# Performance work log

Measured on AMD Instinct MI355X. Metric: run time of the kernel, lower is better.

Reference implementation:

```python
import jax, jax.numpy as jnp
import numpy as np

D_EMB = 256
SCALE = 0.02
B, T = 4, 4096
EPS = 1e-5


def layer_norm(x, w, b):
    m = jnp.mean(x, axis=-1, keepdims=True)
    v = jnp.mean((x - m) ** 2, axis=-1, keepdims=True)
    return (x - m) * jax.lax.rsqrt(v + EPS) * w + b


def setup_inputs() -> dict:
    key = jax.random.key(0)
    ks = jax.random.split(key, 4)
    x = jax.random.normal(ks[0], (B, T, D_EMB), dtype=jnp.float32)
    qkv = jax.random.normal(ks[1], (3, D_EMB, D_EMB), dtype=jnp.float32) * SCALE
    # nn.Linear(D, 2D, bias=False): weight shape (2D, D), applied as x @ W.T
    w1 = jax.random.normal(ks[2], (2 * D_EMB, D_EMB), dtype=jnp.float32) * (1.0 / np.sqrt(D_EMB))
    w2 = jax.random.normal(ks[3], (D_EMB, 2 * D_EMB), dtype=jnp.float32) * (1.0 / np.sqrt(2 * D_EMB))
    ones = jnp.ones((D_EMB,), dtype=jnp.float32)
    zeros = jnp.zeros((D_EMB,), dtype=jnp.float32)
    return {
        "x": x, "qkv": qkv,
        "ln_q_w": ones, "ln_q_b": zeros,
        "ln_k_w": ones, "ln_k_b": zeros,
        "ln_attn_w": ones, "ln_attn_b": zeros,
        "w1": w1, "w2": w2,
        "ln_ff_w": ones, "ln_ff_b": zeros,
    }


def reference(x, qkv, ln_q_w, ln_q_b, ln_k_w, ln_k_b, ln_attn_w, ln_attn_b, w1, w2, ln_ff_w, ln_ff_b):
    # QKV projections: [3, B, T, D]
    y = jnp.einsum('btd,ndD->nbtD', x, qkv)
    q, k, v = y[0], y[1], y[2]
    q = layer_norm(q, ln_q_w, ln_q_b)
    k = layer_norm(k, ln_k_w, ln_k_b)
    # full (non-causal) single-head attention, scale by sqrt(D_EMB)
    scores = jnp.einsum('btd,bsd->bts', q, k) / jnp.sqrt(jnp.float32(D_EMB))
    attn = jax.nn.softmax(scores, axis=-1)
    y = jnp.einsum('bts,bsd->btd', attn, v)
    y = layer_norm(y, ln_attn_w, ln_attn_b)
    x = 0.7 * (x + y)
    # FFN with dual leaky_relu
    y = jax.nn.leaky_relu(x @ w1.T, negative_slope=0.2)
    y = jax.nn.leaky_relu(y @ w2.T, negative_slope=0.2)
    y = layer_norm(y, ln_ff_w, ln_ff_b)
    return 0.7 * (x + y)
```

## Files before the change

### kernel.cpp

```cpp
#include <hip/hip_runtime.h>

#define BSZ   4
#define TSEQ  4096
#define DEMB  256
#define NTOK  (BSZ * TSEQ)
#define HID   512
#define SPLITS 4
#define KEYS_PER_SPLIT (TSEQ / SPLITS)
#define TK 32
#define NT (KEYS_PER_SPLIT / TK)
#define KIMG_STRIDE 8704
#define VIMG_STRIDE 10240

using bf16x8 = __attribute__((ext_vector_type(8))) short;
using f32x16 = __attribute__((ext_vector_type(16))) float;

static __device__ __forceinline__ unsigned short f2bf(float f) {
  union { float f; unsigned u; } v; v.f = f;
  unsigned r = v.u + 0x7FFF + ((v.u >> 16) & 1);
  return (unsigned short)(r >> 16);
}
static __device__ __forceinline__ float bf2f(unsigned short u) {
  union { unsigned u; float f; } v; v.u = ((unsigned)u) << 16;
  return v.f;
}

static __device__ __forceinline__ void async16(void* lds, const void* gp) {
  __builtin_amdgcn_global_load_lds(
      (const __attribute__((address_space(1))) unsigned int*)gp,
      (__attribute__((address_space(3))) unsigned int*)lds, 16, 0, 0);
}

__global__ __launch_bounds__(256) void prep_kernel(
    const float* __restrict__ qkv, const float* __restrict__ w1,
    const float* __restrict__ w2, unsigned short* __restrict__ qkvT,
    unsigned short* __restrict__ w1b, unsigned short* __restrict__ w2b)
{
  const int tid = threadIdx.x;
  if (blockIdx.y < 3) {
    if (blockIdx.x >= 16) return;
    __shared__ float Ts[64][65];
    const int z  = blockIdx.y;
    const int k0 = (blockIdx.x >> 2) * 64;
    const int j0 = (blockIdx.x & 3) * 64;
    const float* src = qkv + (size_t)z * DEMB * DEMB + (size_t)k0 * DEMB + j0;
#pragma unroll
    for (int p = 0; p < 4; ++p) {
      int idx = p * 256 + tid;
      int r = idx >> 4, g = idx & 15;
      float4 v = *(const float4*)(src + (size_t)r * DEMB + g * 4);
      Ts[r][g * 4 + 0] = v.x; Ts[r][g * 4 + 1] = v.y;
      Ts[r][g * 4 + 2] = v.z; Ts[r][g * 4 + 3] = v.w;
    }
    __syncthreads();
    unsigned short* dst = qkvT + (size_t)z * DEMB * DEMB + (size_t)j0 * DEMB + k0;
#pragma unroll
    for (int p = 0; p < 4; ++p) {
      int idx = p * 256 + tid;
      int r = idx >> 4, g = idx & 15;
      ushort4 o;
      o.x = f2bf(Ts[g * 4 + 0][r]); o.y = f2bf(Ts[g * 4 + 1][r]);
      o.z = f2bf(Ts[g * 4 + 2][r]); o.w = f2bf(Ts[g * 4 + 3][r]);
      *(ushort4*)(dst + (size_t)r * DEMB + g * 4) = o;
    }
  } else {
    const float* s = (blockIdx.y == 3) ? w1 : w2;
    unsigned short* d = (blockIdx.y == 3) ? w1b : w2b;
    const int i = blockIdx.x * 256 + tid;
    float4 v = ((const float4*)s)[i];
    ushort4 o;
    o.x = f2bf(v.x); o.y = f2bf(v.y); o.z = f2bf(v.z); o.w = f2bf(v.w);
    ((ushort4*)d)[i] = o;
  }
}

__global__ __launch_bounds__(512, 1) void qkvln_kernel(
    const float* __restrict__ x, const unsigned short* __restrict__ qkvT,
    const float* __restrict__ lnqw, const float* __restrict__ lnqb,
    const float* __restrict__ lnkw, const float* __restrict__ lnkb,
    unsigned short* __restrict__ Qbn, unsigned short* __restrict__ Kimg,
    unsigned short* __restrict__ Vimg)
{
  __shared__ __align__(16) unsigned short sh[36864];
  unsigned short* As = sh;
  unsigned short* Bs = sh + 256 * 72;

  const int tid = threadIdx.x;
  const int w   = tid >> 6;
  const int l   = tid & 63;
  const int lm  = l & 31;
  const int lh  = l >> 5;
  const int z   = blockIdx.y;
  const int m0  = blockIdx.x * 256;
  const int bb  = m0 >> 12;

  const unsigned short* Bt = qkvT + (size_t)z * DEMB * DEMB;

  f32x16 o[8];
#pragma unroll
  for (int t = 0; t < 8; ++t)
#pragma unroll
    for (int r = 0; r < 16; ++r) o[t][r] = 0.f;

  const int fr = tid >> 4;
  const int fc = (tid & 15) * 4;

  float4 arf[8];
  bf16x8 brb[4];

#pragma unroll
  for (int i = 0; i < 8; ++i)
    arf[i] = *(const float4*)(x + (size_t)(m0 + fr + 32 * i) * DEMB + fc);
#pragma unroll
  for (int i = 0; i < 4; ++i) {
    const int c = tid + 512 * i;
    brb[i] = *(const bf16x8*)(Bt + (size_t)(c >> 3) * DEMB + (c & 7) * 8);
  }

  for (int k0 = 0; k0 < DEMB; k0 += 64) {
    __syncthreads();
#pragma unroll
    for (int i = 0; i < 8; ++i) {
      ushort4 u;
      u.x = f2bf(arf[i].x); u.y = f2bf(arf[i].y);
      u.z = f2bf(arf[i].z); u.w = f2bf(arf[i].w);
      *(ushort4*)&As[(fr + 32 * i) * 72 + fc] = u;
    }
#pragma unroll
    for (int i = 0; i < 4; ++i) {
      const int c = tid + 512 * i;
      *(bf16x8*)&Bs[(c >> 3) * 72 + (c & 7) * 8] = brb[i];
    }
    __syncthreads();

    if (k0 + 64 < DEMB) {
      const int kn = k0 + 64;
#pragma unroll
      for (int i = 0; i < 8; ++i)
        arf[i] = *(const float4*)(x + (size_t)(m0 + fr + 32 * i) * DEMB + kn + fc);
#pragma unroll
      for (int i = 0; i < 4; ++i) {
        const int c = tid + 512 * i;
        brb[i] = *(const bf16x8*)(Bt + (size_t)(c >> 3) * DEMB + kn + (c & 7) * 8);
      }
    }

#pragma unroll
    for (int ks = 0; ks < 4; ++ks) {
      bf16x8 a = *(const bf16x8*)&As[(w * 32 + lm) * 72 + ks * 16 + lh * 8];
#pragma unroll
      for (int t = 0; t < 8; ++t) {
        bf16x8 b = *(const bf16x8*)&Bs[(t * 32 + lm) * 72 + ks * 16 + lh * 8];
        o[t] = __builtin_amdgcn_mfma_f32_32x32x16_bf16(a, b, o[t], 0, 0, 0);
      }
    }
  }

  __syncthreads();

  if (z < 2) {
    const float* wp = z ? lnkw : lnqw;
    const float* bp = z ? lnkb : lnqb;
    float wc[8], bc[8];
#pragma unroll
    for (int t = 0; t < 8; ++t) { wc[t] = wp[t * 32 + lm]; bc[t] = bp[t * 32 + lm]; }
#pragma unroll
    for (int r = 0; r < 16; ++r) {
      float sv = 0.f, sq = 0.f;
#pragma unroll
      for (int t = 0; t < 8; ++t) { const float v = o[t][r]; sv += v; sq += v * v; }
#pragma unroll
      for (int d = 1; d < 32; d <<= 1) { sv += __shfl_xor(sv, d, 64); sq += __shfl_xor(sq, d, 64); }
      const float mean = sv * (1.f / DEMB);
      const float rs = rsqrtf(sq * (1.f / DEMB) - mean * mean + 1e-5f);
      const int token = m0 + w * 32 + (r & 3) + 8 * (r >> 2) + 4 * lh;
      if (z == 0) {
        unsigned short* dst = Qbn + (size_t)token * DEMB;
#pragma unroll
        for (int t = 0; t < 8; ++t)
          dst[t * 32 + lm] = f2bf((o[t][r] - mean) * rs * wc[t] + bc[t]);
      } else {
        const int t5 = token & 4095;
        unsigned short* dst =
            Kimg + (size_t)(bb * 128 + (t5 >> 5)) * KIMG_STRIDE + (t5 & 31) * 264;
#pragma unroll
        for (int t = 0; t < 8; ++t)
          dst[t * 32 + lm] = f2bf((o[t][r] - mean) * rs * wc[t] + bc[t]);
      }
    }
  } else {
#pragma unroll
    for (int h = 0; h < 2; ++h) {
      if (h) __syncthreads();
#pragma unroll
      for (int t2 = 0; t2 < 4; ++t2) {
        const int t = h * 4 + t2;
#pragma unroll
        for (int r = 0; r < 16; ++r) {
          const int row = w * 32 + (r & 3) + 8 * (r >> 2) + 4 * lh;
          sh[row * 130 + t2 * 32 + lm] = f2bf(o[t][r]);
        }
      }
      __syncthreads();
      const int d2 = tid & 127;
      const int tq = tid >> 7;
      const int d  = h * 128 + d2;
#pragma unroll
      for (int j = 0; j < 16; ++j) {
        const int tok0 = tq * 64 + j * 4;
        ushort4 v;
        v.x = sh[(tok0 + 0) * 130 + d2];
        v.y = sh[(tok0 + 1) * 130 + d2];
        v.z = sh[(tok0 + 2) * 130 + d2];
        v.w = sh[(tok0 + 3) * 130 + d2];
        const int gtok = m0 + tok0;
        const int kt = (gtok & 4095) >> 5;
        *(ushort4*)(Vimg + (size_t)(bb * 128 + kt) * VIMG_STRIDE + d * 40 + (tok0 & 31)) = v;
      }
    }
  }
}

__global__ __launch_bounds__(256, 3) void gemm_ffn_kernel(
    const unsigned short* __restrict__ A, const unsigned short* __restrict__ Bt,
    unsigned short* __restrict__ C, int M, int N, int K)
{
  __shared__ __align__(16) unsigned short As[128 * 72];
  __shared__ __align__(16) unsigned short Bs[128 * 72];

  const int tid = threadIdx.x;
  const int w   = tid >> 6;
  const int wm  = w >> 1, wn = w & 1;
  const int l   = tid & 63;
  const int lm  = l & 31;
  const int lh  = l >> 5;

  const int m0    = blockIdx.x * 128;
  const int nbase = blockIdx.y * 128;

  f32x16 acc00, acc01, acc10, acc11;
#pragma unroll
  for (int r = 0; r < 16; ++r) { acc00[r] = 0.f; acc01[r] = 0.f; acc10[r] = 0.f; acc11[r] = 0.f; }

  const int lr = tid >> 3;
  const int lc = (tid & 7) * 8;

  bf16x8 arb[4], brb[4];

#pragma unroll
  for (int i = 0; i < 4; ++i) {
    arb[i] = *(const bf16x8*)(A  + (size_t)(m0 + i * 32 + lr) * K + lc);
    brb[i] = *(const bf16x8*)(Bt + (size_t)(nbase + i * 32 + lr) * K + lc);
  }

  for (int k0 = 0; k0 < K; k0 += 64) {
    __syncthreads();
#pragma unroll
    for (int i = 0; i < 4; ++i) {
      *(bf16x8*)&As[(i * 32 + lr) * 72 + lc] = arb[i];
      *(bf16x8*)&Bs[(i * 32 + lr) * 72 + lc] = brb[i];
    }
    __syncthreads();

    if (k0 + 64 < K) {
      const int kn = k0 + 64;
#pragma unroll
      for (int i = 0; i < 4; ++i) {
        arb[i] = *(const bf16x8*)(A  + (size_t)(m0 + i * 32 + lr) * K + kn + lc);
        brb[i] = *(const bf16x8*)(Bt + (size_t)(nbase + i * 32 + lr) * K + kn + lc);
      }
    }

#pragma unroll
    for (int ks = 0; ks < 4; ++ks) {
      bf16x8 a0 = *(const bf16x8*)&As[(wm * 64 + lm)      * 72 + ks * 16 + lh * 8];
      bf16x8 a1 = *(const bf16x8*)&As[(wm * 64 + 32 + lm) * 72 + ks * 16 + lh * 8];
      bf16x8 b0 = *(const bf16x8*)&Bs[(wn * 64 + lm)      * 72 + ks * 16 + lh * 8];
      bf16x8 b1 = *(const bf16x8*)&Bs[(wn * 64 + 32 + lm) * 72 + ks * 16 + lh * 8];
      acc00 = __builtin_amdgcn_mfma_f32_32x32x16_bf16(a0, b0, acc00, 0, 0, 0);
      acc01 = __builtin_amdgcn_mfma_f32_32x32x16_bf16(a0, b1, acc01, 0, 0, 0);
      acc10 = __builtin_amdgcn_mfma_f32_32x32x16_bf16(a1, b0, acc10, 0, 0, 0);
      acc11 = __builtin_amdgcn_mfma_f32_32x32x16_bf16(a1, b1, acc11, 0, 0, 0);
    }
  }

  const f32x16* accs[4] = { &acc00, &acc01, &acc10, &acc11 };
#pragma unroll
  for (int am = 0; am < 2; ++am)
#pragma unroll
    for (int bn = 0; bn < 2; ++bn) {
      const f32x16& a = *accs[am * 2 + bn];
#pragma unroll
      for (int r = 0; r < 16; ++r) {
        const int m = m0 + wm * 64 + am * 32 + (r & 3) + 8 * (r >> 2) + 4 * lh;
        const int n = nbase + wn * 64 + bn * 32 + lm;
        float v = a[r];
        v = v > 0.f ? v : 0.2f * v;
        C[(size_t)m * N + n] = f2bf(v);
      }
    }
}

__global__ __launch_bounds__(256) void ln_res_bf16_kernel(
    const unsigned short* __restrict__ Y, const float* __restrict__ Xin,
    const float* __restrict__ w, const float* __restrict__ b,
    float* __restrict__ Out)
{
  const int lane = threadIdx.x & 63;
  const size_t row = (size_t)blockIdx.x * 4 + (threadIdx.x >> 6);
  ushort4 u = *(const ushort4*)&Y[row * DEMB + lane * 4];
  float y0 = bf2f(u.x), y1 = bf2f(u.y), y2 = bf2f(u.z), y3 = bf2f(u.w);
  float s  = y0 + y1 + y2 + y3;
  float sq = y0 * y0 + y1 * y1 + y2 * y2 + y3 * y3;
#pragma unroll
  for (int o = 32; o > 0; o >>= 1) { s += __shfl_down(s, o); sq += __shfl_down(sq, o); }
  s = __shfl(s, 0); sq = __shfl(sq, 0);
  const float m  = s * (1.f / DEMB);
  const float rs = rsqrtf(sq * (1.f / DEMB) - m * m + 1e-5f);
  const float4 wv = *(const float4*)&w[lane * 4];
  const float4 bv = *(const float4*)&b[lane * 4];
  const float4 xi = *(const float4*)&Xin[row * DEMB + lane * 4];
  float4 o;
  o.x = 0.7f * (xi.x + (y0 - m) * rs * wv.x + bv.x);
  o.y = 0.7f * (xi.y + (y1 - m) * rs * wv.y + bv.y);
  o.z = 0.7f * (xi.z + (y2 - m) * rs * wv.z + bv.z);
  o.w = 0.7f * (xi.w + (y3 - m) * rs * wv.w + bv.w);
  *(float4*)&Out[row * DEMB + lane * 4] = o;
}

__global__ __launch_bounds__(512) void attn_split_kernel(
    const unsigned short* __restrict__ Qb, const unsigned short* __restrict__ Kimg,
    const unsigned short* __restrict__ Vimg, unsigned short* __restrict__ Opart,
    float* __restrict__ lpart)
{
  __shared__ __align__(16) unsigned short Ks[2][KIMG_STRIDE];
  __shared__ __align__(16) unsigned short Vs[3][VIMG_STRIDE];
  __shared__ __align__(16) unsigned short Pb[8 * 32 * 40];

  const int tid = threadIdx.x;
  const int w   = tid >> 6;
  const int l   = tid & 63;
  const int lm  = l & 31;
  const int lh  = l >> 5;

  const int lin = blockIdx.x;
  const int xcd = lin & 7;
  const int idx = lin >> 3;
  const int b     = xcd >> 1;
  const int split = (xcd & 1) * 2 + (idx & 1);
  const int q0    = (idx >> 1) * 256;

  const unsigned short* Qbase  = Qb + (size_t)b * TSEQ * DEMB;
  const unsigned short* Ktiles = Kimg + (size_t)(b * 128 + split * 32) * KIMG_STRIDE;
  const unsigned short* Vtiles = Vimg + (size_t)(b * 128 + split * 32) * VIMG_STRIDE;

  bf16x8 qf[16];
  {
    const unsigned short* qrow = Qbase + (size_t)(q0 + w * 32 + lm) * DEMB + lh * 8;
#pragma unroll
    for (int ks = 0; ks < 16; ++ks) qf[ks] = *(const bf16x8*)(qrow + ks * 16);
  }

  f32x16 o[8];
  float lsum[16], spv[16];
#pragma unroll
  for (int t = 0; t < 8; ++t)
#pragma unroll
    for (int r = 0; r < 16; ++r) o[t][r] = 0.f;
#pragma unroll
  for (int r = 0; r < 16; ++r) lsum[r] = 0.f;

  unsigned short* Pw = &Pb[w * 32 * 40];

#pragma unroll
  for (int i = 0; i < 3; ++i) {
    const int c = w + 8 * i;
    if (c < 17) async16(&Ks[0][c * 512], Ktiles + c * 512 + l * 8);
  }
#pragma unroll
  for (int i = 0; i < 3; ++i) {
    const int c = w + 8 * i;
    if (c < 20) async16(&Vs[0][c * 512], Vtiles + c * 512 + l * 8);
  }

  {
    __syncthreads();
#pragma unroll
    for (int i = 0; i < 3; ++i) {
      const int c = w + 8 * i;
      if (c < 17) async16(&Ks[1][c * 512], Ktiles + (size_t)KIMG_STRIDE + c * 512 + l * 8);
    }
#pragma unroll
    for (int i = 0; i < 3; ++i) {
      const int c = w + 8 * i;
      if (c < 20) async16(&Vs[1][c * 512], Vtiles + (size_t)VIMG_STRIDE + c * 512 + l * 8);
    }
    f32x16 s;
#pragma unroll
    for (int r = 0; r < 16; ++r) s[r] = 0.f;
#pragma unroll
    for (int ks = 0; ks < 16; ++ks) {
      bf16x8 kf = *(const bf16x8*)&Ks[0][lm * 264 + ks * 16 + lh * 8];
      s = __builtin_amdgcn_mfma_f32_32x32x16_bf16(qf[ks], kf, s, 0, 0, 0);
    }
#pragma unroll
    for (int r = 0; r < 16; ++r) spv[r] = s[r];
  }

  int vprev = 0, vcur = 1, vnext = 2;

  for (int st = 1; st < NT; ++st) {
    __syncthreads();

    if (st + 1 < NT) {
      const unsigned short* kn = Ktiles + (size_t)(st + 1) * KIMG_STRIDE;
      const unsigned short* vn = Vtiles + (size_t)(st + 1) * VIMG_STRIDE;
#pragma unroll
      for (int i = 0; i < 3; ++i) {
        const int c = w + 8 * i;
        if (c < 17) async16(&Ks[(st + 1) & 1][c * 512], kn + c * 512 + l * 8);
      }
#pragma unroll
      for (int i = 0; i < 3; ++i) {
        const int c = w + 8 * i;
        if (c < 20) async16(&Vs[vnext][c * 512], vn + c * 512 + l * 8);
      }
    }

#pragma unroll
    for (int r = 0; r < 16; ++r) {
      const float pv = exp2f(spv[r] * 0.09016844335f - 11.541560327f);
      lsum[r] += pv;
      const int row = (r & 3) + ((r >> 2) << 3) + (lh << 2);
      Pw[row * 40 + lm] = f2bf(pv);
    }
    {
      const unsigned short* Vp = &Vs[vprev][0];
#pragma unroll
      for (int ks = 0; ks < 2; ++ks) {
        bf16x8 pf = *(const bf16x8*)&Pw[lm * 40 + ks * 16 + lh * 8];
#pragma unroll
        for (int t = 0; t < 8; ++t) {
          bf16x8 vf = *(const bf16x8*)&Vp[(t * 32 + lm) * 40 + ks * 16 + lh * 8];
          o[t] = __builtin_amdgcn_mfma_f32_32x32x16_bf16(pf, vf, o[t], 0, 0, 0);
        }
      }
    }

    {
      f32x16 s;
#pragma unroll
      for (int r = 0; r < 16; ++r) s[r] = 0.f;
      const unsigned short* Kp = &Ks[st & 1][0];
#pragma unroll
      for (int ks = 0; ks < 16; ++ks) {
        bf16x8 kf = *(const bf16x8*)&Kp[lm * 264 + ks * 16 + lh * 8];
        s = __builtin_amdgcn_mfma_f32_32x32x16_bf16(qf[ks], kf, s, 0, 0, 0);
      }
#pragma unroll
      for (int r = 0; r < 16; ++r) spv[r] = s[r];
    }

    const int tmp = vprev; vprev = vcur; vcur = vnext; vnext = tmp;
  }

#pragma unroll
  for (int r = 0; r < 16; ++r) {
    const float pv = exp2f(spv[r] * 0.09016844335f - 11.541560327f);
    lsum[r] += pv;
    const int row = (r & 3) + ((r >> 2) << 3) + (lh << 2);
    Pw[row * 40 + lm] = f2bf(pv);
  }
  {
    const unsigned short* Vp = &Vs[vprev][0];
#pragma unroll
    for (int ks = 0; ks < 2; ++ks) {
      bf16x8 pf = *(const bf16x8*)&Pw[lm * 40 + ks * 16 + lh * 8];
#pragma unroll
      for (int t = 0; t < 8; ++t) {
        bf16x8 vf = *(const bf16x8*)&Vp[(t * 32 + lm) * 40 + ks * 16 + lh * 8];
        o[t] = __builtin_amdgcn_mfma_f32_32x32x16_bf16(pf, vf, o[t], 0, 0, 0);
      }
    }
  }

#pragma unroll
  for (int r = 0; r < 16; ++r) {
#pragma unroll
    for (int d = 1; d < 32; d <<= 1) lsum[r] += __shfl_xor(lsum[r], d, 64);
  }
  unsigned short* Ob =
      Opart + ((size_t)split * NTOK + (size_t)b * TSEQ + q0 + w * 32) * DEMB;
  float* lb = lpart + (size_t)split * NTOK + (size_t)b * TSEQ + q0 + w * 32;
#pragma unroll
  for (int r = 0; r < 16; ++r) {
    const int row = (r & 3) + ((r >> 2) << 3) + (lh << 2);
#pragma unroll
    for (int t = 0; t < 8; ++t)
      Ob[(size_t)row * DEMB + t * 32 + lm] = f2bf(o[t][r]);
    if (lm == 0) lb[row] = lsum[r];
  }
}

__global__ __launch_bounds__(256) void combine_lnres_kernel(
    const unsigned short* __restrict__ Opart, const float* __restrict__ lpart,
    const float* __restrict__ Xin, const float* __restrict__ w,
    const float* __restrict__ b, float* __restrict__ Out,
    unsigned short* __restrict__ Outb)
{
  const int lane = threadIdx.x & 63;
  const size_t row = (size_t)blockIdx.x * 4 + (threadIdx.x >> 6);
  float4 acc = make_float4(0.f, 0.f, 0.f, 0.f);
  float lt = 0.f;
#pragma unroll
  for (int p = 0; p < SPLITS; ++p) {
    const ushort4 u = *(const ushort4*)&Opart[((size_t)p * NTOK + row) * DEMB + lane * 4];
    acc.x += bf2f(u.x); acc.y += bf2f(u.y);
    acc.z += bf2f(u.z); acc.w += bf2f(u.w);
    lt += lpart[(size_t)p * NTOK + row];
  }
  const float inv = 1.f / lt;
  const float y0 = acc.x * inv, y1 = acc.y * inv, y2 = acc.z * inv, y3 = acc.w * inv;
  float s  = y0 + y1 + y2 + y3;
  float sq = y0 * y0 + y1 * y1 + y2 * y2 + y3 * y3;
#pragma unroll
  for (int o = 32; o > 0; o >>= 1) { s += __shfl_down(s, o); sq += __shfl_down(sq, o); }
  s = __shfl(s, 0); sq = __shfl(sq, 0);
  const float m  = s * (1.f / DEMB);
  const float rs = rsqrtf(sq * (1.f / DEMB) - m * m + 1e-5f);
  const float4 wv = *(const float4*)&w[lane * 4];
  const float4 bv = *(const float4*)&b[lane * 4];
  const float4 xi = *(const float4*)&Xin[row * DEMB + lane * 4];
  float4 o;
  o.x = 0.7f * (xi.x + (y0 - m) * rs * wv.x + bv.x);
  o.y = 0.7f * (xi.y + (y1 - m) * rs * wv.y + bv.y);
  o.z = 0.7f * (xi.z + (y2 - m) * rs * wv.z + bv.z);
  o.w = 0.7f * (xi.w + (y3 - m) * rs * wv.w + bv.w);
  *(float4*)&Out[row * DEMB + lane * 4] = o;
  ushort4 ob;
  ob.x = f2bf(o.x); ob.y = f2bf(o.y); ob.z = f2bf(o.z); ob.w = f2bf(o.w);
  *(ushort4*)&Outb[row * DEMB + lane * 4] = ob;
}

extern "C" void kernel_launch(void* const* d_in, const int* in_sizes, int n_in,
                              void* d_out, int out_size, void* d_ws, size_t ws_size,
                              hipStream_t stream)
{
  (void)in_sizes; (void)n_in; (void)out_size; (void)ws_size;
  const float* x    = (const float*)d_in[0];
  const float* qkv  = (const float*)d_in[1];
  const float* lnqw = (const float*)d_in[2];
  const float* lnqb = (const float*)d_in[3];
  const float* lnkw = (const float*)d_in[4];
  const float* lnkb = (const float*)d_in[5];
  const float* lnaw = (const float*)d_in[6];
  const float* lnab = (const float*)d_in[7];
  const float* w1   = (const float*)d_in[8];
  const float* w2   = (const float*)d_in[9];
  const float* lnfw = (const float*)d_in[10];
  const float* lnfb = (const float*)d_in[11];
  float* out = (float*)d_out;

  char* W = (char*)d_ws;
  const size_t MB = 1 << 20;
  unsigned short* Qbn   = (unsigned short*)(W + 0);
  unsigned short* Kimg  = (unsigned short*)(W + 8 * MB);
  unsigned short* Vimg  = (unsigned short*)(W + 17 * MB);
  unsigned short* Opart = (unsigned short*)(W + 28 * MB);
  float*          lpart = (float*)(W + 60 * MB);
  unsigned short* x1b   = (unsigned short*)(W + 0);
  unsigned short* H     = (unsigned short*)(W + 8 * MB);
  unsigned short* Y2b   = (unsigned short*)(W + 28 * MB);
  unsigned short* qkvT  = (unsigned short*)(W + 60 * MB + 512 * 1024);
  unsigned short* w1b   = (unsigned short*)(W + 61 * MB);
  unsigned short* w2b   = (unsigned short*)(W + 61 * MB + 256 * 1024);

  const dim3 blk(256);

  prep_kernel<<<dim3(128, 5), blk, 0, stream>>>(qkv, w1, w2, qkvT, w1b, w2b);

  qkvln_kernel<<<dim3(NTOK / 256, 3), dim3(512), 0, stream>>>(
      x, qkvT, lnqw, lnqb, lnkw, lnkb, Qbn, Kimg, Vimg);

  attn_split_kernel<<<dim3(256), dim3(512), 0, stream>>>(Qbn, Kimg, Vimg, Opart, lpart);
  combine_lnres_kernel<<<NTOK / 4, blk, 0, stream>>>(Opart, lpart, x, lnaw, lnab, out, x1b);

  gemm_ffn_kernel<<<dim3(NTOK / 128, HID / 128), blk, 0, stream>>>(
      x1b, w1b, H, NTOK, HID, DEMB);
  gemm_ffn_kernel<<<dim3(NTOK / 128, DEMB / 128), blk, 0, stream>>>(
      H, w2b, Y2b, NTOK, DEMB, HID);

  ln_res_bf16_kernel<<<NTOK / 4, blk, 0, stream>>>(Y2b, out, lnfw, lnfb, out);
}
```

Measured before the change: 228.0 us.

## Retile QKV projection to 128-row blocks and keep residual intermediate in bf16

The QKV+LayerNorm kernel now uses 128-token tiles with 256 threads and two blocks per CU. This doubles the grid so the CUs are filled more evenly. The attention combine kernel no longer writes the fp32 post-attention residual to the output. The final LayerNorm-residual kernel reads the bf16 copy instead, which cuts global-memory traffic. In exchange the second residual add uses bf16-rounded inputs, which lowers accuracy.

```diff
diff --git a/kernel.cpp b/kernel.cpp
--- a/kernel.cpp
+++ b/kernel.cpp
@@ -74,16 +74,16 @@
   }
 }
 
-__global__ __launch_bounds__(512, 1) void qkvln_kernel(
+__global__ __launch_bounds__(256, 2) void qkvln_kernel(
     const float* __restrict__ x, const unsigned short* __restrict__ qkvT,
     const float* __restrict__ lnqw, const float* __restrict__ lnqb,
     const float* __restrict__ lnkw, const float* __restrict__ lnkb,
     unsigned short* __restrict__ Qbn, unsigned short* __restrict__ Kimg,
     unsigned short* __restrict__ Vimg)
 {
-  __shared__ __align__(16) unsigned short sh[36864];
+  __shared__ __align__(16) unsigned short sh[128 * 72 + 256 * 72];
   unsigned short* As = sh;
-  unsigned short* Bs = sh + 256 * 72;
+  unsigned short* Bs = sh + 128 * 72;
 
   const int tid = threadIdx.x;
   const int w   = tid >> 6;
@@ -91,7 +91,7 @@
   const int lm  = l & 31;
   const int lh  = l >> 5;
   const int z   = blockIdx.y;
-  const int m0  = blockIdx.x * 256;
+  const int m0  = blockIdx.x * 128;
   const int bb  = m0 >> 12;
 
   const unsigned short* Bt = qkvT + (size_t)z * DEMB * DEMB;
@@ -102,46 +102,35 @@
 #pragma unroll
     for (int r = 0; r < 16; ++r) o[t][r] = 0.f;
 
-  const int fr = tid >> 4;
-  const int fc = (tid & 15) * 4;
-
   float4 arf[8];
-  bf16x8 brb[4];
-
-#pragma unroll
-  for (int i = 0; i < 8; ++i)
-    arf[i] = *(const float4*)(x + (size_t)(m0 + fr + 32 * i) * DEMB + fc);
-#pragma unroll
-  for (int i = 0; i < 4; ++i) {
-    const int c = tid + 512 * i;
-    brb[i] = *(const bf16x8*)(Bt + (size_t)(c >> 3) * DEMB + (c & 7) * 8);
+  bf16x8 brb[8];
+#pragma unroll
+  for (int i = 0; i < 8; ++i) {
+    const int ia = i * 256 + tid;
+    arf[i] = *(const float4*)(x + (size_t)(m0 + (ia >> 4)) * DEMB + (ia & 15) * 4);
+    brb[i] = *(const bf16x8*)(Bt + (size_t)(ia >> 3) * DEMB + (ia & 7) * 8);
   }
 
   for (int k0 = 0; k0 < DEMB; k0 += 64) {
     __syncthreads();
 #pragma unroll
     for (int i = 0; i < 8; ++i) {
+      const int ia = i * 256 + tid;
       ushort4 u;
       u.x = f2bf(arf[i].x); u.y = f2bf(arf[i].y);
       u.z = f2bf(arf[i].z); u.w = f2bf(arf[i].w);
-      *(ushort4*)&As[(fr + 32 * i) * 72 + fc] = u;
-    }
-#pragma unroll
-    for (int i = 0; i < 4; ++i) {
-      const int c = tid + 512 * i;
-      *(bf16x8*)&Bs[(c >> 3) * 72 + (c & 7) * 8] = brb[i];
+      *(ushort4*)&As[(ia >> 4) * 72 + (ia & 15) * 4] = u;
+      *(bf16x8*)&Bs[(ia >> 3) * 72 + (ia & 7) * 8] = brb[i];
     }
     __syncthreads();
 
     if (k0 + 64 < DEMB) {
       const int kn = k0 + 64;
 #pragma unroll
-      for (int i = 0; i < 8; ++i)
-        arf[i] = *(const float4*)(x + (size_t)(m0 + fr + 32 * i) * DEMB + kn + fc);
-#pragma unroll
-      for (int i = 0; i < 4; ++i) {
-        const int c = tid + 512 * i;
-        brb[i] = *(const bf16x8*)(Bt + (size_t)(c >> 3) * DEMB + kn + (c & 7) * 8);
+      for (int i = 0; i < 8; ++i) {
+        const int ia = i * 256 + tid;
+        arf[i] = *(const float4*)(x + (size_t)(m0 + (ia >> 4)) * DEMB + kn + (ia & 15) * 4);
+        brb[i] = *(const bf16x8*)(Bt + (size_t)(ia >> 3) * DEMB + kn + (ia & 7) * 8);
       }
     }
 
@@ -155,8 +144,6 @@
       }
     }
   }
-
-  __syncthreads();
 
   if (z < 2) {
     const float* wp = z ? lnkw : lnqw;
@@ -191,7 +178,7 @@
   } else {
 #pragma unroll
     for (int h = 0; h < 2; ++h) {
-      if (h) __syncthreads();
+      __syncthreads();
 #pragma unroll
       for (int t2 = 0; t2 < 4; ++t2) {
         const int t = h * 4 + t2;
@@ -301,8 +288,8 @@
     }
 }
 
-__global__ __launch_bounds__(256) void ln_res_bf16_kernel(
-    const unsigned short* __restrict__ Y, const float* __restrict__ Xin,
+__global__ __launch_bounds__(256) void ln_res_bf16x_kernel(
+    const unsigned short* __restrict__ Y, const unsigned short* __restrict__ X1,
     const float* __restrict__ w, const float* __restrict__ b,
     float* __restrict__ Out)
 {
@@ -310,6 +297,216 @@
   const size_t row = (size_t)blockIdx.x * 4 + (threadIdx.x >> 6);
   ushort4 u = *(const ushort4*)&Y[row * DEMB + lane * 4];
   float y0 = bf2f(u.x), y1 = bf2f(u.y), y2 = bf2f(u.z), y3 = bf2f(u.w);
+  float s  = y0 + y1 + y2 + y3;
+  float sq = y0 * y0 + y1 * y1 + y2 * y2 + y3 * y3;
+#pragma unroll
+  for (int o = 32; o > 0; o >>= 1) { s += __shfl_down(s, o); sq += __shfl_down(sq, o); }
+  s = __shfl(s, 0); sq = __shfl(sq, 0);
+  const float m  = s * (1.f / DEMB);
+  const float rs = rsqrtf(sq * (1.f / DEMB) - m * m + 1e-5f);
+  const float4 wv = *(const float4*)&w[lane * 4];
+  const float4 bv = *(const float4*)&b[lane * 4];
+  const ushort4 xu = *(const ushort4*)&X1[row * DEMB + lane * 4];
+  float4 o;
+  o.x = 0.7f * (bf2f(xu.x) + (y0 - m) * rs * wv.x + bv.x);
+  o.y = 0.7f * (bf2f(xu.y) + (y1 - m) * rs * wv.y + bv.y);
+  o.z = 0.7f * (bf2f(xu.z) + (y2 - m) * rs * wv.z + bv.z);
+  o.w = 0.7f * (bf2f(xu.w) + (y3 - m) * rs * wv.w + bv.w);
+  *(float4*)&Out[row * DEMB + lane * 4] = o;
+}
+
+__global__ __launch_bounds__(512) void attn_split_kernel(
+    const unsigned short* __restrict__ Qb, const unsigned short* __restrict__ Kimg,
+    const unsigned short* __restrict__ Vimg, unsigned short* __restrict__ Opart,
+    float* __restrict__ lpart)
+{
+  __shared__ __align__(16) unsigned short Ks[2][KIMG_STRIDE];
+  __shared__ __align__(16) unsigned short Vs[3][VIMG_STRIDE];
+  __shared__ __align__(16) unsigned short Pb[8 * 32 * 40];
+
+  const int tid = threadIdx.x;
+  const int w   = tid >> 6;
+  const int l   = tid & 63;
+  const int lm  = l & 31;
+  const int lh  = l >> 5;
+
+  const int lin = blockIdx.x;
+  const int xcd = lin & 7;
+  const int idx = lin >> 3;
+  const int b     = xcd >> 1;
+  const int split = (xcd & 1) * 2 + (idx & 1);
+  const int q0    = (idx >> 1) * 256;
+
+  const unsigned short* Qbase  = Qb + (size_t)b * TSEQ * DEMB;
+  const unsigned short* Ktiles = Kimg + (size_t)(b * 128 + split * 32) * KIMG_STRIDE;
+  const unsigned short* Vtiles = Vimg + (size_t)(b * 128 + split * 32) * VIMG_STRIDE;
+
+  bf16x8 qf[16];
+  {
+    const unsigned short* qrow = Qbase + (size_t)(q0 + w * 32 + lm) * DEMB + lh * 8;
+#pragma unroll
+    for (int ks = 0; ks < 16; ++ks) qf[ks] = *(const bf16x8*)(qrow + ks * 16);
+  }
+
+  f32x16 o[8];
+  float lsum[16], spv[16];
+#pragma unroll
+  for (int t = 0; t < 8; ++t)
+#pragma unroll
+    for (int r = 0; r < 16; ++r) o[t][r] = 0.f;
+#pragma unroll
+  for (int r = 0; r < 16; ++r) lsum[r] = 0.f;
+
+  unsigned short* Pw = &Pb[w * 32 * 40];
+
+#pragma unroll
+  for (int i = 0; i < 3; ++i) {
+    const int c = w + 8 * i;
+    if (c < 17) async16(&Ks[0][c * 512], Ktiles + c * 512 + l * 8);
+  }
+#pragma unroll
+  for (int i = 0; i < 3; ++i) {
+    const int c = w + 8 * i;
+    if (c < 20) async16(&Vs[0][c * 512], Vtiles + c * 512 + l * 8);
+  }
+
+  {
+    __syncthreads();
+#pragma unroll
+    for (int i = 0; i < 3; ++i) {
+      const int c = w + 8 * i;
+      if (c < 17) async16(&Ks[1][c * 512], Ktiles + (size_t)KIMG_STRIDE + c * 512 + l * 8);
+    }
+#pragma unroll
+    for (int i = 0; i < 3; ++i) {
+      const int c = w + 8 * i;
+      if (c < 20) async16(&Vs[1][c * 512], Vtiles + (size_t)VIMG_STRIDE + c * 512 + l * 8);
+    }
+    f32x16 s;
+#pragma unroll
+    for (int r = 0; r < 16; ++r) s[r] = 0.f;
+#pragma unroll
+    for (int ks = 0; ks < 16; ++ks) {
+      bf16x8 kf = *(const bf16x8*)&Ks[0][lm * 264 + ks * 16 + lh * 8];
+      s = __builtin_amdgcn_mfma_f32_32x32x16_bf16(qf[ks], kf, s, 0, 0, 0);
+    }
+#pragma unroll
+    for (int r = 0; r < 16; ++r) spv[r] = s[r];
+  }
+
+  int vprev = 0, vcur = 1, vnext = 2;
+
+  for (int st = 1; st < NT; ++st) {
+    __syncthreads();
+
+    if (st + 1 < NT) {
+      const unsigned short* kn = Ktiles + (size_t)(st + 1) * KIMG_STRIDE;
+      const unsigned short* vn = Vtiles + (size_t)(st + 1) * VIMG_STRIDE;
+#pragma unroll
+      for (int i = 0; i < 3; ++i) {
+        const int c = w + 8 * i;
+        if (c < 17) async16(&Ks[(st + 1) & 1][c * 512], kn + c * 512 + l * 8);
+      }
+#pragma unroll
+      for (int i = 0; i < 3; ++i) {
+        const int c = w + 8 * i;
+        if (c < 20) async16(&Vs[vnext][c * 512], vn + c * 512 + l * 8);
+      }
+    }
+
+#pragma unroll
+    for (int r = 0; r < 16; ++r) {
+      const float pv = exp2f(spv[r] * 0.09016844335f - 11.541560327f);
+      lsum[r] += pv;
+      const int row = (r & 3) + ((r >> 2) << 3) + (lh << 2);
+      Pw[row * 40 + lm] = f2bf(pv);
+    }
+    {
+      const unsigned short* Vp = &Vs[vprev][0];
+#pragma unroll
+      for (int ks = 0; ks < 2; ++ks) {
+        bf16x8 pf = *(const bf16x8*)&Pw[lm * 40 + ks * 16 + lh * 8];
+#pragma unroll
+        for (int t = 0; t < 8; ++t) {
+          bf16x8 vf = *(const bf16x8*)&Vp[(t * 32 + lm) * 40 + ks * 16 + lh * 8];
+          o[t] = __builtin_amdgcn_mfma_f32_32x32x16_bf16(pf, vf, o[t], 0, 0, 0);
+        }
+      }
+    }
+
+    {
+      f32x16 s;
+#pragma unroll
+      for (int r = 0; r < 16; ++r) s[r] = 0.f;
+      const unsigned short* Kp = &Ks[st & 1][0];
+#pragma unroll
+      for (int ks = 0; ks < 16; ++ks) {
+        bf16x8 kf = *(const bf16x8*)&Kp[lm * 264 + ks * 16 + lh * 8];
+        s = __builtin_amdgcn_mfma_f32_32x32x16_bf16(qf[ks], kf, s, 0, 0, 0);
+      }
+#pragma unroll
+      for (int r = 0; r < 16; ++r) spv[r] = s[r];
+    }
+
+    const int tmp = vprev; vprev = vcur; vcur = vnext; vnext = tmp;
+  }
+
+#pragma unroll
+  for (int r = 0; r < 16; ++r) {
+    const float pv = exp2f(spv[r] * 0.09016844335f - 11.541560327f);
+    lsum[r] += pv;
+    const int row = (r & 3) + ((r >> 2) << 3) + (lh << 2);
+    Pw[row * 40 + lm] = f2bf(pv);
+  }
+  {
+    const unsigned short* Vp = &Vs[vprev][0];
+#pragma unroll
+    for (int ks = 0; ks < 2; ++ks) {
+      bf16x8 pf = *(const bf16x8*)&Pw[lm * 40 + ks * 16 + lh * 8];
+#pragma unroll
+      for (int t = 0; t < 8; ++t) {
+        bf16x8 vf = *(const bf16x8*)&Vp[(t * 32 + lm) * 40 + ks * 16 + lh * 8];
+        o[t] = __builtin_amdgcn_mfma_f32_32x32x16_bf16(pf, vf, o[t], 0, 0, 0);
+      }
+    }
+  }
+
+#pragma unroll
+  for (int r = 0; r < 16; ++r) {
+#pragma unroll
+    for (int d = 1; d < 32; d <<= 1) lsum[r] += __shfl_xor(lsum[r], d, 64);
+  }
+  unsigned short* Ob =
+      Opart + ((size_t)split * NTOK + (size_t)b * TSEQ + q0 + w * 32) * DEMB;
+  float* lb = lpart + (size_t)split * NTOK + (size_t)b * TSEQ + q0 + w * 32;
+#pragma unroll
+  for (int r = 0; r < 16; ++r) {
+    const int row = (r & 3) + ((r >> 2) << 3) + (lh << 2);
+#pragma unroll
+    for (int t = 0; t < 8; ++t)
+      Ob[(size_t)row * DEMB + t * 32 + lm] = f2bf(o[t][r]);
+    if (lm == 0) lb[row] = lsum[r];
+  }
+}
+
+__global__ __launch_bounds__(256) void combine_lnres_kernel(
+    const unsigned short* __restrict__ Opart, const float* __restrict__ lpart,
+    const float* __restrict__ Xin, const float* __restrict__ w,
+    const float* __restrict__ b, unsigned short* __restrict__ Outb)
+{
+  const int lane = threadIdx.x & 63;
+  const size_t row = (size_t)blockIdx.x * 4 + (threadIdx.x >> 6);
+  float4 acc = make_float4(0.f, 0.f, 0.f, 0.f);
+  float lt = 0.f;
+#pragma unroll
+  for (int p = 0; p < SPLITS; ++p) {
+    const ushort4 u = *(const ushort4*)&Opart[((size_t)p * NTOK + row) * DEMB + lane * 4];
+    acc.x += bf2f(u.x); acc.y += bf2f(u.y);
+    acc.z += bf2f(u.z); acc.w += bf2f(u.w);
+    lt += lpart[(size_t)p * NTOK + row];
+  }
+  const float inv = 1.f / lt;
+  const float y0 = acc.x * inv, y1 = acc.y * inv, y2 = acc.z * inv, y3 = acc.w * inv;
   float s  = y0 + y1 + y2 + y3;
   float sq = y0 * y0 + y1 * y1 + y2 * y2 + y3 * y3;
 #pragma unroll
@@ -320,225 +517,11 @@
   const float4 wv = *(const float4*)&w[lane * 4];
   const float4 bv = *(const float4*)&b[lane * 4];
   const float4 xi = *(const float4*)&Xin[row * DEMB + lane * 4];
-  float4 o;
-  o.x = 0.7f * (xi.x + (y0 - m) * rs * wv.x + bv.x);
-  o.y = 0.7f * (xi.y + (y1 - m) * rs * wv.y + bv.y);
-  o.z = 0.7f * (xi.z + (y2 - m) * rs * wv.z + bv.z);
-  o.w = 0.7f * (xi.w + (y3 - m) * rs * wv.w + bv.w);
-  *(float4*)&Out[row * DEMB + lane * 4] = o;
-}
-
-__global__ __launch_bounds__(512) void attn_split_kernel(
-    const unsigned short* __restrict__ Qb, const unsigned short* __restrict__ Kimg,
-    const unsigned short* __restrict__ Vimg, unsigned short* __restrict__ Opart,
-    float* __restrict__ lpart)
-{
-  __shared__ __align__(16) unsigned short Ks[2][KIMG_STRIDE];
-  __shared__ __align__(16) unsigned short Vs[3][VIMG_STRIDE];
-  __shared__ __align__(16) unsigned short Pb[8 * 32 * 40];
-
-  const int tid = threadIdx.x;
-  const int w   = tid >> 6;
-  const int l   = tid & 63;
-  const int lm  = l & 31;
-  const int lh  = l >> 5;
-
-  const int lin = blockIdx.x;
-  const int xcd = lin & 7;
-  const int idx = lin >> 3;
-  const int b     = xcd >> 1;
-  const int split = (xcd & 1) * 2 + (idx & 1);
-  const int q0    = (idx >> 1) * 256;
-
-  const unsigned short* Qbase  = Qb + (size_t)b * TSEQ * DEMB;
-  const unsigned short* Ktiles = Kimg + (size_t)(b * 128 + split * 32) * KIMG_STRIDE;
-  const unsigned short* Vtiles = Vimg + (size_t)(b * 128 + split * 32) * VIMG_STRIDE;
-
-  bf16x8 qf[16];
-  {
-    const unsigned short* qrow = Qbase + (size_t)(q0 + w * 32 + lm) * DEMB + lh * 8;
-#pragma unroll
-    for (int ks = 0; ks < 16; ++ks) qf[ks] = *(const bf16x8*)(qrow + ks * 16);
-  }
-
-  f32x16 o[8];
-  float lsum[16], spv[16];
-#pragma unroll
-  for (int t = 0; t < 8; ++t)
-#pragma unroll
-    for (int r = 0; r < 16; ++r) o[t][r] = 0.f;
-#pragma unroll
-  for (int r = 0; r < 16; ++r) lsum[r] = 0.f;
-
-  unsigned short* Pw = &Pb[w * 32 * 40];
-
-#pragma unroll
-  for (int i = 0; i < 3; ++i) {
-    const int c = w + 8 * i;
-    if (c < 17) async16(&Ks[0][c * 512], Ktiles + c * 512 + l * 8);
-  }
-#pragma unroll
-  for (int i = 0; i < 3; ++i) {
-    const int c = w + 8 * i;
-    if (c < 20) async16(&Vs[0][c * 512], Vtiles + c * 512 + l * 8);
-  }
-
-  {
-    __syncthreads();
-#pragma unroll
-    for (int i = 0; i < 3; ++i) {
-      const int c = w + 8 * i;
-      if (c < 17) async16(&Ks[1][c * 512], Ktiles + (size_t)KIMG_STRIDE + c * 512 + l * 8);
-    }
-#pragma unroll
-    for (int i = 0; i < 3; ++i) {
-      const int c = w + 8 * i;
-      if (c < 20) async16(&Vs[1][c * 512], Vtiles + (size_t)VIMG_STRIDE + c * 512 + l * 8);
-    }
-    f32x16 s;
-#pragma unroll
-    for (int r = 0; r < 16; ++r) s[r] = 0.f;
-#pragma unroll
-    for (int ks = 0; ks < 16; ++ks) {
-      bf16x8 kf = *(const bf16x8*)&Ks[0][lm * 264 + ks * 16 + lh * 8];
-      s = __builtin_amdgcn_mfma_f32_32x32x16_bf16(qf[ks], kf, s, 0, 0, 0);
-    }
-#pragma unroll
-    for (int r = 0; r < 16; ++r) spv[r] = s[r];
-  }
-
-  int vprev = 0, vcur = 1, vnext = 2;
-
-  for (int st = 1; st < NT; ++st) {
-    __syncthreads();
-
-    if (st + 1 < NT) {
-      const unsigned short* kn = Ktiles + (size_t)(st + 1) * KIMG_STRIDE;
-      const unsigned short* vn = Vtiles + (size_t)(st + 1) * VIMG_STRIDE;
-#pragma unroll
-      for (int i = 0; i < 3; ++i) {
-        const int c = w + 8 * i;
-        if (c < 17) async16(&Ks[(st + 1) & 1][c * 512], kn + c * 512 + l * 8);
-      }
-#pragma unroll
-      for (int i = 0; i < 3; ++i) {
-        const int c = w + 8 * i;
-        if (c < 20) async16(&Vs[vnext][c * 512], vn + c * 512 + l * 8);
-      }
-    }
-
-#pragma unroll
-    for (int r = 0; r < 16; ++r) {
-      const float pv = exp2f(spv[r] * 0.09016844335f - 11.541560327f);
-      lsum[r] += pv;
-      const int row = (r & 3) + ((r >> 2) << 3) + (lh << 2);
-      Pw[row * 40 + lm] = f2bf(pv);
-    }
-    {
-      const unsigned short* Vp = &Vs[vprev][0];
-#pragma unroll
-      for (int ks = 0; ks < 2; ++ks) {
-        bf16x8 pf = *(const bf16x8*)&Pw[lm * 40 + ks * 16 + lh * 8];
-#pragma unroll
-        for (int t = 0; t < 8; ++t) {
-          bf16x8 vf = *(const bf16x8*)&Vp[(t * 32 + lm) * 40 + ks * 16 + lh * 8];
-          o[t] = __builtin_amdgcn_mfma_f32_32x32x16_bf16(pf, vf, o[t], 0, 0, 0);
-        }
-      }
-    }
-
-    {
-      f32x16 s;
-#pragma unroll
-      for (int r = 0; r < 16; ++r) s[r] = 0.f;
-      const unsigned short* Kp = &Ks[st & 1][0];
-#pragma unroll
-      for (int ks = 0; ks < 16; ++ks) {
-        bf16x8 kf = *(const bf16x8*)&Kp[lm * 264 + ks * 16 + lh * 8];
-        s = __builtin_amdgcn_mfma_f32_32x32x16_bf16(qf[ks], kf, s, 0, 0, 0);
-      }
-#pragma unroll
-      for (int r = 0; r < 16; ++r) spv[r] = s[r];
-    }
-
-    const int tmp = vprev; vprev = vcur; vcur = vnext; vnext = tmp;
-  }
-
-#pragma unroll
-  for (int r = 0; r < 16; ++r) {
-    const float pv = exp2f(spv[r] * 0.09016844335f - 11.541560327f);
-    lsum[r] += pv;
-    const int row = (r & 3) + ((r >> 2) << 3) + (lh << 2);
-    Pw[row * 40 + lm] = f2bf(pv);
-  }
-  {
-    const unsigned short* Vp = &Vs[vprev][0];
-#pragma unroll
-    for (int ks = 0; ks < 2; ++ks) {
-      bf16x8 pf = *(const bf16x8*)&Pw[lm * 40 + ks * 16 + lh * 8];
-#pragma unroll
-      for (int t = 0; t < 8; ++t) {
-        bf16x8 vf = *(const bf16x8*)&Vp[(t * 32 + lm) * 40 + ks * 16 + lh * 8];
-        o[t] = __builtin_amdgcn_mfma_f32_32x32x16_bf16(pf, vf, o[t], 0, 0, 0);
-      }
-    }
-  }
-
-#pragma unroll
-  for (int r = 0; r < 16; ++r) {
-#pragma unroll
-    for (int d = 1; d < 32; d <<= 1) lsum[r] += __shfl_xor(lsum[r], d, 64);
-  }
-  unsigned short* Ob =
-      Opart + ((size_t)split * NTOK + (size_t)b * TSEQ + q0 + w * 32) * DEMB;
-  float* lb = lpart + (size_t)split * NTOK + (size_t)b * TSEQ + q0 + w * 32;
-#pragma unroll
-  for (int r = 0; r < 16; ++r) {
-    const int row = (r & 3) + ((r >> 2) << 3) + (lh << 2);
-#pragma unroll
-    for (int t = 0; t < 8; ++t)
-      Ob[(size_t)row * DEMB + t * 32 + lm] = f2bf(o[t][r]);
-    if (lm == 0) lb[row] = lsum[r];
-  }
-}
-
-__global__ __launch_bounds__(256) void combine_lnres_kernel(
-    const unsigned short* __restrict__ Opart, const float* __restrict__ lpart,
-    const float* __restrict__ Xin, const float* __restrict__ w,
-    const float* __restrict__ b, float* __restrict__ Out,
-    unsigned short* __restrict__ Outb)
-{
-  const int lane = threadIdx.x & 63;
-  const size_t row = (size_t)blockIdx.x * 4 + (threadIdx.x >> 6);
-  float4 acc = make_float4(0.f, 0.f, 0.f, 0.f);
-  float lt = 0.f;
-#pragma unroll
-  for (int p = 0; p < SPLITS; ++p) {
-    const ushort4 u = *(const ushort4*)&Opart[((size_t)p * NTOK + row) * DEMB + lane * 4];
-    acc.x += bf2f(u.x); acc.y += bf2f(u.y);
-    acc.z += bf2f(u.z); acc.w += bf2f(u.w);
-    lt += lpart[(size_t)p * NTOK + row];
-  }
-  const float inv = 1.f / lt;
-  const float y0 = acc.x * inv, y1 = acc.y * inv, y2 = acc.z * inv, y3 = acc.w * inv;
-  float s  = y0 + y1 + y2 + y3;
-  float sq = y0 * y0 + y1 * y1 + y2 * y2 + y3 * y3;
-#pragma unroll
-  for (int o = 32; o > 0; o >>= 1) { s += __shfl_down(s, o); sq += __shfl_down(sq, o); }
-  s = __shfl(s, 0); sq = __shfl(sq, 0);
-  const float m  = s * (1.f / DEMB);
-  const float rs = rsqrtf(sq * (1.f / DEMB) - m * m + 1e-5f);
-  const float4 wv = *(const float4*)&w[lane * 4];
-  const float4 bv = *(const float4*)&b[lane * 4];
-  const float4 xi = *(const float4*)&Xin[row * DEMB + lane * 4];
-  float4 o;
-  o.x = 0.7f * (xi.x + (y0 - m) * rs * wv.x + bv.x);
-  o.y = 0.7f * (xi.y + (y1 - m) * rs * wv.y + bv.y);
-  o.z = 0.7f * (xi.z + (y2 - m) * rs * wv.z + bv.z);
-  o.w = 0.7f * (xi.w + (y3 - m) * rs * wv.w + bv.w);
-  *(float4*)&Out[row * DEMB + lane * 4] = o;
   ushort4 ob;
-  ob.x = f2bf(o.x); ob.y = f2bf(o.y); ob.z = f2bf(o.z); ob.w = f2bf(o.w);
+  ob.x = f2bf(0.7f * (xi.x + (y0 - m) * rs * wv.x + bv.x));
+  ob.y = f2bf(0.7f * (xi.y + (y1 - m) * rs * wv.y + bv.y));
+  ob.z = f2bf(0.7f * (xi.z + (y2 - m) * rs * wv.z + bv.z));
+  ob.w = f2bf(0.7f * (xi.w + (y3 - m) * rs * wv.w + bv.w));
   *(ushort4*)&Outb[row * DEMB + lane * 4] = ob;
 }
 
@@ -567,28 +550,28 @@
   unsigned short* Kimg  = (unsigned short*)(W + 8 * MB);
   unsigned short* Vimg  = (unsigned short*)(W + 17 * MB);
   unsigned short* Opart = (unsigned short*)(W + 28 * MB);
-  float*          lpart = (float*)(W + 60 * MB);
+  float*          lpart = (float*)(W + 62 * MB);
   unsigned short* x1b   = (unsigned short*)(W + 0);
   unsigned short* H     = (unsigned short*)(W + 8 * MB);
   unsigned short* Y2b   = (unsigned short*)(W + 28 * MB);
-  unsigned short* qkvT  = (unsigned short*)(W + 60 * MB + 512 * 1024);
-  unsigned short* w1b   = (unsigned short*)(W + 61 * MB);
-  unsigned short* w2b   = (unsigned short*)(W + 61 * MB + 256 * 1024);
+  unsigned short* qkvT  = (unsigned short*)(W + 62 * MB + 512 * 1024);
+  unsigned short* w1b   = (unsigned short*)(W + 63 * MB);
+  unsigned short* w2b   = (unsigned short*)(W + 63 * MB + 256 * 1024);
 
   const dim3 blk(256);
 
   prep_kernel<<<dim3(128, 5), blk, 0, stream>>>(qkv, w1, w2, qkvT, w1b, w2b);
 
-  qkvln_kernel<<<dim3(NTOK / 256, 3), dim3(512), 0, stream>>>(
+  qkvln_kernel<<<dim3(NTOK / 128, 3), blk, 0, stream>>>(
       x, qkvT, lnqw, lnqb, lnkw, lnkb, Qbn, Kimg, Vimg);
 
   attn_split_kernel<<<dim3(256), dim3(512), 0, stream>>>(Qbn, Kimg, Vimg, Opart, lpart);
-  combine_lnres_kernel<<<NTOK / 4, blk, 0, stream>>>(Opart, lpart, x, lnaw, lnab, out, x1b);
+  combine_lnres_kernel<<<NTOK / 4, blk, 0, stream>>>(Opart, lpart, x, lnaw, lnab, x1b);
 
   gemm_ffn_kernel<<<dim3(NTOK / 128, HID / 128), blk, 0, stream>>>(
       x1b, w1b, H, NTOK, HID, DEMB);
   gemm_ffn_kernel<<<dim3(NTOK / 128, DEMB / 128), blk, 0, stream>>>(
       H, w2b, Y2b, NTOK, DEMB, HID);
 
-  ln_res_bf16_kernel<<<NTOK / 4, blk, 0, stream>>>(Y2b, out, lnfw, lnfb, out);
-}
+  ln_res_bf16x_kernel<<<NTOK / 4, blk, 0, stream>>>(Y2b, x1b, lnfw, lnfb, out);
+}
```

Result: no change. 229.5 us (+0.6%).
